# Performance work log

Measured on AMD Instinct MI355X. Metric: run time of the kernel, lower is better.

## Reference

```python
import jax, jax.numpy as jnp
import numpy as np

N_HEADS = 16
HEAD_DIM = 64
ATTN_WINDOW = 128
ROPE_BASE = 10000.0


def _rotate_half(x):
    # (x0, x1) -> (-x1, x0) over interleaved pairs in the last dim
    xr = x.reshape(*x.shape[:-1], -1, 2)
    out = jnp.stack((-xr[..., 1], xr[..., 0]), axis=-1)
    return out.reshape(x.shape)


def _rope_cos_sin(T, rotary_dim, base, dtype):
    inv_freq = 1.0 / (base ** (jnp.arange(0, rotary_dim, 2, dtype=jnp.float32) / rotary_dim))
    t = jnp.arange(T, dtype=jnp.float32)
    freqs = t[:, None] * inv_freq[None, :]            # (T, rotary_dim/2)
    cos = jnp.repeat(jnp.cos(freqs), 2, axis=-1)      # (T, rotary_dim)
    sin = jnp.repeat(jnp.sin(freqs), 2, axis=-1)
    return cos.astype(dtype), sin.astype(dtype)


def _apply_rope(x, cos, sin):
    # x: (B, H, T, Dh); rotary_dim == Dh here (rope_fraction = 1.0)
    c = cos[None, None, :, :]
    s = sin[None, None, :, :]
    return x * c + _rotate_half(x) * s


def setup_inputs() -> dict:
    key = jax.random.key(0)
    ks = jax.random.split(key, 5)
    B, T, C = 2, 2048, 1024
    x = jax.random.normal(ks[0], (B, T, C), dtype=jnp.float32)
    Wqkv = jax.random.normal(ks[1], (C, 3 * C), dtype=jnp.float32) * 0.02
    bqkv = jax.random.normal(ks[2], (3 * C,), dtype=jnp.float32) * 0.02
    Wproj = jax.random.normal(ks[3], (C, C), dtype=jnp.float32) * 0.02
    bproj = jax.random.normal(ks[4], (C,), dtype=jnp.float32) * 0.02
    return {"x": x, "Wqkv": Wqkv, "bqkv": bqkv, "Wproj": Wproj, "bproj": bproj}


def reference(x, Wqkv, bqkv, Wproj, bproj):
    B, T, C = x.shape
    H, Dh = N_HEADS, HEAD_DIM

    qkv = x @ Wqkv + bqkv                              # (B, T, 3C)
    q, k, v = jnp.split(qkv, 3, axis=-1)

    def heads(t):
        return t.reshape(B, T, H, Dh).transpose(0, 2, 1, 3)  # (B, H, T, Dh)
    q, k, v = heads(q), heads(k), heads(v)

    cos, sin = _rope_cos_sin(T, Dh, ROPE_BASE, x.dtype)
    q = _apply_rope(q, cos, sin)
    k = _apply_rope(k, cos, sin)

    # local causal mask: allowed iff 0 <= i - j < attn_window
    idx = jnp.arange(T)
    rel = idx[:, None] - idx[None, :]
    allowed = (rel >= 0) & (rel < ATTN_WINDOW)         # (T, T)

    scale = 1.0 / jnp.sqrt(jnp.asarray(Dh, dtype=x.dtype))
    scores = jnp.einsum("bhqd,bhkd->bhqk", q, k) * scale
    scores = jnp.where(allowed[None, None], scores, jnp.asarray(-jnp.inf, dtype=x.dtype))
    attn = jax.nn.softmax(scores, axis=-1)
    attn_out = jnp.einsum("bhqk,bhkd->bhqd", attn, v)  # (B, H, T, Dh)

    attn_out = attn_out.transpose(0, 2, 1, 3).reshape(B, T, C)
    return attn_out @ Wproj + bproj
```

## Files before the change

kernel.cpp:

```cpp
#include <hip/hip_runtime.h>


using bf16x8 = short  __attribute__((ext_vector_type(8)));
using f32x4  = float __attribute__((ext_vector_type(4)));

__device__ __forceinline__ float bf2f(unsigned short u) {
    return __uint_as_float(((unsigned int)u) << 16);
}
__device__ __forceinline__ unsigned short f2bf(float f) {
    unsigned int u = __float_as_uint(f);
    u += 0x7fffu + ((u >> 16) & 1u);
    return (unsigned short)(u >> 16);
}

__device__ __forceinline__ void gload_lds16(const unsigned short* g,
                                            unsigned short* l) {
    __builtin_amdgcn_global_load_lds(
        (const __attribute__((address_space(1))) unsigned int*)(g),
        (__attribute__((address_space(3))) unsigned int*)(l),
        16, 0, 0);
}

template <int N>
__device__ __forceinline__ void vm_wait() {
    static_assert(N == 0 || N == 2 || N == 3 || N == 4 || N == 6, "add case");
    if constexpr (N == 0)      asm volatile("s_waitcnt vmcnt(0)" ::: "memory");
    else if constexpr (N == 2) asm volatile("s_waitcnt vmcnt(2)" ::: "memory");
    else if constexpr (N == 3) asm volatile("s_waitcnt vmcnt(3)" ::: "memory");
    else if constexpr (N == 4) asm volatile("s_waitcnt vmcnt(4)" ::: "memory");
    else                       asm volatile("s_waitcnt vmcnt(6)" ::: "memory");
}
__device__ __forceinline__ void lgkm_wait0() {
    asm volatile("s_waitcnt lgkmcnt(0)" ::: "memory");
}

__global__ __launch_bounds__(256) void prep_kernel(
        const float* __restrict__ Wqkv, const float* __restrict__ Wproj,
        const float* __restrict__ x,
        unsigned short* __restrict__ WqkvT, unsigned short* __restrict__ WprojT,
        unsigned short* __restrict__ xb, float* __restrict__ tab) {
    __shared__ unsigned short tile[32][33];
    int blk = blockIdx.x;
    int tid = threadIdx.x;
    if (blk < 4096) {
        const float* W; unsigned short* WT; int cols, bx, by;
        if (blk < 3072) { W = Wqkv;  WT = WqkvT;  cols = 3072; bx = blk % 96; by = blk / 96; }
        else            { W = Wproj; WT = WprojT; cols = 1024; bx = (blk - 3072) & 31; by = (blk - 3072) >> 5; }
        int c0 = bx * 32, r0 = by * 32;
        int tx = tid & 31, ty = tid >> 5;
        for (int i = ty; i < 32; i += 8)
            tile[i][tx] = f2bf(W[(size_t)(r0 + i) * cols + c0 + tx]);
        __syncthreads();
        for (int i = ty; i < 32; i += 8)
            WT[(size_t)(c0 + i) * 1024 + r0 + tx] = tile[tx][i];
    } else if (blk < 5120) {
        for (int i = (blk - 4096) * 256 + tid; i < 1048576; i += 262144) {
            float4 v = ((const float4*)x)[i];
            ushort4 o;
            o.x = f2bf(v.x); o.y = f2bf(v.y); o.z = f2bf(v.z); o.w = f2bf(v.w);
            ((ushort4*)xb)[i] = o;
        }
    } else {
        int idx = (blk - 5120) * 256 + tid;
        int t = idx >> 5, i = idx & 31;
        float inv = powf(10000.0f, -(float)i / 32.0f);
        float ang = (float)t * inv;
        tab[idx * 2]     = cosf(ang);
        tab[idx * 2 + 1] = sinf(ang);
    }
}

template <int BM, int BN, int WM, int WN, bool OUT_BF16, bool FUSE_ROPE, int DEPTH>
__global__ __launch_bounds__(256) void gemm_lds(
        const unsigned short* __restrict__ A,
        const unsigned short* __restrict__ Bt,
        const float* __restrict__ bias,
        void* __restrict__ Cv,
        const float* __restrict__ tab,
        int M, int N, int K) {
    constexpr int MI = BM / 16;
    constexpr int NI = BN / 16;
    constexpr int PW = (MI + NI) / 4;
    constexpr int WGN = BN / WN;
    constexpr int MR = WM / 16, NR = WN / 16;

    __shared__ unsigned short smem[DEPTH * (BM + BN) * 32];
    auto As = [&](int buf) { return &smem[buf * (BM + BN) * 32]; };
    auto Bs = [&](int buf) { return &smem[buf * (BM + BN) * 32 + BM * 32]; };

    int nwg = gridDim.x * gridDim.y;
    int lid = blockIdx.y * gridDim.x + blockIdx.x;
    int orig = (lid & 7) * (nwg >> 3) + (lid >> 3);
    int bx = orig % gridDim.x, by = orig / gridDim.x;

    int row0 = by * BM, col0 = bx * BN;
    int tid = threadIdx.x;
    int lane = tid & 63, wid = tid >> 6;
    int wr = wid / WGN, wc = wid % WGN;
    int fr = lane & 15, kq = lane >> 4;
    int r_in = lane >> 2;
    int scg8 = (((lane & 3) ^ ((lane >> 3) & 3))) * 8;
    int kqs8 = (kq ^ ((fr >> 1) & 3)) * 8;

    f32x4 acc[MR][NR];
    #pragma unroll
    for (int i = 0; i < MR; ++i)
        #pragma unroll
        for (int j = 0; j < NR; ++j)
            acc[i][j] = (f32x4){0.f, 0.f, 0.f, 0.f};

    auto stage = [&](int buf, int kt) {
        #pragma unroll
        for (int t = 0; t < PW; ++t) {
            int j = wid * PW + t;
            if (j < MI) {
                int row = j * 16 + r_in;
                gload_lds16(A + (size_t)(row0 + row) * K + kt + scg8,
                            As(buf) + j * 512);
            } else {
                int jb = j - MI;
                int row = jb * 16 + r_in;
                gload_lds16(Bt + (size_t)(col0 + row) * K + kt + scg8,
                            Bs(buf) + jb * 512);
            }
        }
    };
    auto compute = [&](int buf) {
        bf16x8 af[MR], bfv[NR];
        #pragma unroll
        for (int i = 0; i < MR; ++i)
            af[i] = *(const bf16x8*)&As(buf)[(wr * WM + i * 16 + fr) * 32 + kqs8];
        #pragma unroll
        for (int j = 0; j < NR; ++j)
            bfv[j] = *(const bf16x8*)&Bs(buf)[(wc * WN + j * 16 + fr) * 32 + kqs8];
        #pragma unroll
        for (int i = 0; i < MR; ++i)
            #pragma unroll
            for (int j = 0; j < NR; ++j)
                acc[i][j] = __builtin_amdgcn_mfma_f32_16x16x32_bf16(
                                af[i], bfv[j], acc[i][j], 0, 0, 0);
    };

    int nt = K >> 5;
    stage(0, 0);
    if constexpr (DEPTH == 3) stage(1, 32);
    int cc = 0;
    int cs = DEPTH - 1;
    for (int t = 0; t < nt; ++t) {
        int rem = nt - 1 - t;
        if (rem >= DEPTH - 1) {
            stage(cs, (t + DEPTH - 1) << 5);
            vm_wait<(DEPTH - 1) * PW>();
        } else if (rem == 1) {
            vm_wait<PW>();
        } else {
            vm_wait<0>();
        }
        __builtin_amdgcn_s_barrier();
        compute(cc);
        if (t + 1 < nt) {
            lgkm_wait0();
            __builtin_amdgcn_s_barrier();
        }
        cc = (cc + 1 == DEPTH) ? 0 : cc + 1;
        cs = (cs + 1 == DEPTH) ? 0 : cs + 1;
    }

    int rg = kq * 4;
    if constexpr (OUT_BF16) {
        static_assert(BM * BN <= DEPTH * (BM + BN) * 32, "epilogue tile must fit");
        unsigned short* Ct = smem;
        __syncthreads();
        #pragma unroll
        for (int j = 0; j < NR; ++j) {
            int colL = wc * WN + j * 16 + fr;
            float bz = bias[col0 + colL];
            #pragma unroll
            for (int i = 0; i < MR; ++i) {
                float v4[4];
                #pragma unroll
                for (int r = 0; r < 4; ++r) v4[r] = acc[i][j][r] + bz;
                if constexpr (FUSE_ROPE) {
                    if (col0 < 2048) {
                        int ii2 = (colL & 63) >> 1;
                        bool odd = fr & 1;
                        #pragma unroll
                        for (int r = 0; r < 4; ++r) {
                            float part = __shfl_xor(v4[r], 1);
                            int trow = (row0 + wr * WM + i * 16 + rg + r) & 2047;
                            float cc2 = tab[(trow * 32 + ii2) * 2];
                            float ss = tab[(trow * 32 + ii2) * 2 + 1];
                            v4[r] = odd ? fmaf(v4[r], cc2,  part * ss)
                                        : fmaf(v4[r], cc2, -part * ss);
                        }
                    }
                }
                #pragma unroll
                for (int r = 0; r < 4; ++r)
                    Ct[(wr * WM + i * 16 + rg + r) * BN + colL] = f2bf(v4[r]);
            }
        }
        __syncthreads();
        unsigned short* C = (unsigned short*)Cv;
        constexpr int ROUNDS = (BM * BN / 8) / 256;
        #pragma unroll
        for (int p = 0; p < ROUNDS; ++p) {
            int idx = p * 256 + tid;
            int row = idx / (BN / 8);
            int c8v = (idx % (BN / 8)) * 8;
            *(bf16x8*)&C[(size_t)(row0 + row) * N + col0 + c8v] =
                *(const bf16x8*)&Ct[row * BN + c8v];
        }
    } else {
        float* C = (float*)Cv;
        #pragma unroll
        for (int j = 0; j < NR; ++j) {
            int col = col0 + wc * WN + j * 16 + fr;
            float bz = bias[col];
            #pragma unroll
            for (int i = 0; i < MR; ++i) {
                #pragma unroll
                for (int r = 0; r < 4; ++r) {
                    int row = row0 + wr * WM + i * 16 + rg + r;
                    C[(size_t)row * N + col] = acc[i][j][r] + bz;
                }
            }
        }
    }
}

#define VTS 200
#define PSS 168

__global__ __launch_bounds__(256) void attn_kernel(
        const unsigned short* __restrict__ qkv, unsigned short* __restrict__ aout) {
    __shared__ unsigned short Vt[64 * VTS];
    __shared__ unsigned short Ps[4 * 16 * PSS];

    int bid = blockIdx.x;
    int h  = bid & 15;
    int qt = (bid >> 4) & 31;
    int b  = bid >> 9;
    int Q0 = qt * 64;
    int kbase = Q0 - 127; if (kbase < 0) kbase = 0;
    int nk = Q0 + 64 - kbase;
    int tid = threadIdx.x;

    {
        int r32 = tid & 31;
        int c8  = (tid >> 5) * 8;
        #pragma unroll
        for (int p = 0; p < 7; ++p) {
            int r = p * 32 + r32;
            if (r < VTS) {
                unsigned int wv[4] = {0u, 0u, 0u, 0u};
                if (r < nk) {
                    uint4 v = *(const uint4*)(qkv +
                        (size_t)(b * 2048 + kbase + r) * 3072 + 2048 + h * 64 + c8);
                    wv[0] = v.x; wv[1] = v.y; wv[2] = v.z; wv[3] = v.w;
                }
                #pragma unroll
                for (int j = 0; j < 4; ++j) {
                    Vt[(c8 + 2 * j)     * VTS + r] = (unsigned short)(wv[j] & 0xffffu);
                    Vt[(c8 + 2 * j + 1) * VTS + r] = (unsigned short)(wv[j] >> 16);
                }
            }
        }
    }
    __syncthreads();

    int lane = tid & 63, w = tid >> 6;
    int qw0 = Q0 + w * 16;
    int lo = lane & 15, hi = lane >> 4;

    const unsigned short* qg =
        qkv + (size_t)(b * 2048 + qw0 + lo) * 3072 + h * 64 + hi * 8;
    bf16x8 aq0 = *(const bf16x8*)qg;
    bf16x8 aq1 = *(const bf16x8*)(qg + 32);

    int klo = qw0 - 127; if (klo < kbase) klo = kbase;
    int t0 = (klo - kbase) >> 4;
    int t1 = (qw0 + 15 - kbase) >> 4;
    int ntiles = t1 - t0 + 1;
    if ((ntiles & 1) && t0 > 0) { --t0; ++ntiles; }
    int nks = (ntiles + 1) >> 1;
    int wkb = t0 * 16;

    f32x4 s[10];
    #pragma unroll
    for (int i = 0; i < 10; ++i) s[i] = (f32x4){0.f, 0.f, 0.f, 0.f};
    #pragma unroll
    for (int i = 0; i < 10; ++i) {
        if (i < ntiles) {
            const unsigned short* kg = qkv +
                (size_t)(b * 2048 + kbase + (t0 + i) * 16 + lo) * 3072
                + 1024 + h * 64 + hi * 8;
            bf16x8 bk0 = *(const bf16x8*)kg;
            bf16x8 bk1 = *(const bf16x8*)(kg + 32);
            __builtin_amdgcn_s_setprio(1);
            s[i] = __builtin_amdgcn_mfma_f32_16x16x32_bf16(aq0, bk0, s[i], 0, 0, 0);
            s[i] = __builtin_amdgcn_mfma_f32_16x16x32_bf16(aq1, bk1, s[i], 0, 0, 0);
            __builtin_amdgcn_s_setprio(0);
        }
    }

    const float scale = 0.125f;
    float mx[4] = {-1e30f, -1e30f, -1e30f, -1e30f};
    #pragma unroll
    for (int i = 0; i < 10; ++i) {
        if (i < ntiles) {
            int ka = kbase + (t0 + i) * 16 + lo;
            #pragma unroll
            for (int r = 0; r < 4; ++r) {
                int rel = (qw0 + hi * 4 + r) - ka;
                bool ok = (rel >= 0) && (rel < 128);
                float v = ok ? s[i][r] * scale : -1e30f;
                s[i][r] = v;
                mx[r] = fmaxf(mx[r], v);
            }
        }
    }
    #pragma unroll
    for (int r = 0; r < 4; ++r)
        #pragma unroll
        for (int o = 1; o < 16; o <<= 1)
            mx[r] = fmaxf(mx[r], __shfl_xor(mx[r], o));

    float sum[4] = {0.f, 0.f, 0.f, 0.f};
    #pragma unroll
    for (int i = 0; i < 10; ++i) {
        if (i < ntiles) {
            #pragma unroll
            for (int r = 0; r < 4; ++r) {
                float e = __expf(s[i][r] - mx[r]);
                s[i][r] = e;
                sum[r] += e;
            }
        }
    }
    #pragma unroll
    for (int r = 0; r < 4; ++r) {
        #pragma unroll
        for (int o = 1; o < 16; o <<= 1)
            sum[r] += __shfl_xor(sum[r], o);
        sum[r] = 1.0f / sum[r];
    }

    unsigned short* pw = &Ps[(w * 16) * PSS];
    #pragma unroll
    for (int i = 0; i < 10; ++i) {
        if (i < ntiles) {
            #pragma unroll
            for (int r = 0; r < 4; ++r)
                pw[(hi * 4 + r) * PSS + i * 16 + lo] = f2bf(s[i][r] * sum[r]);
        }
    }
    if (ntiles & 1) {
        int zr = lane >> 2, zc = ntiles * 16 + (lane & 3) * 4;
        *(ushort4*)&pw[zr * PSS + zc] = (ushort4){0, 0, 0, 0};
    }

    f32x4 o[4];
    #pragma unroll
    for (int dt = 0; dt < 4; ++dt) o[dt] = (f32x4){0.f, 0.f, 0.f, 0.f};
    #pragma unroll
    for (int ks = 0; ks < 5; ++ks) {
        if (ks < nks) {
            bf16x8 pa = *(const bf16x8*)&Ps[(w * 16 + lo) * PSS + ks * 32 + hi * 8];
            __builtin_amdgcn_s_setprio(1);
            #pragma unroll
            for (int dt = 0; dt < 4; ++dt) {
                bf16x8 vb = *(const bf16x8*)&Vt[(dt * 16 + lo) * VTS
                                                + wkb + ks * 32 + hi * 8];
                o[dt] = __builtin_amdgcn_mfma_f32_16x16x32_bf16(pa, vb, o[dt], 0, 0, 0);
            }
            __builtin_amdgcn_s_setprio(0);
        }
    }

    #pragma unroll
    for (int dt = 0; dt < 4; ++dt)
        #pragma unroll
        for (int r = 0; r < 4; ++r)
            aout[(size_t)(b * 2048 + qw0 + hi * 4 + r) * 1024
                 + h * 64 + dt * 16 + lo] = f2bf(o[dt][r]);
}

extern "C" void kernel_launch(void* const* d_in, const int* in_sizes, int n_in,
                              void* d_out, int out_size, void* d_ws, size_t ws_size,
                              hipStream_t stream) {
    const float* x     = (const float*)d_in[0];
    const float* Wqkv  = (const float*)d_in[1];
    const float* bqkv  = (const float*)d_in[2];
    const float* Wproj = (const float*)d_in[3];
    const float* bproj = (const float*)d_in[4];
    float* out = (float*)d_out;

    char* ws = (char*)d_ws;
    unsigned short* WqkvT  = (unsigned short*)(ws);
    unsigned short* WprojT = (unsigned short*)(ws + 6291456);
    unsigned short* xb     = (unsigned short*)(ws + 8388608);
    unsigned short* qkv    = (unsigned short*)(ws + 16777216);
    float*          tab    = (float*)        (ws + 41943040);
    unsigned short* attno  = (unsigned short*)(ws + 42467328);

    prep_kernel<<<5376, 256, 0, stream>>>(Wqkv, Wproj, x, WqkvT, WprojT, xb, tab);

    gemm_lds<128, 64, 32, 64, true, true, 2>
        <<<dim3(48, 32), 256, 0, stream>>>(xb, WqkvT, bqkv, qkv, tab, 4096, 3072, 1024);
    attn_kernel<<<1024, 256, 0, stream>>>(qkv, attno);
    gemm_lds<64, 64, 32, 32, false, false, 2>
        <<<dim3(16, 64), 256, 0, stream>>>(attno, WprojT, bproj, out, nullptr, 4096, 1024, 1024);
}
```

Measured before the change: 114.5 us.

## Add direct-A-load 128x128 QKV GEMM and enlarge projection GEMM tiles

Adds a dedicated QKV GEMM kernel with 128x128 tiles. Each wave loads its A fragments straight from global memory into registers, and only B is staged through LDS with double-buffered async loads. This halves the number of QKV workgroups and raises per-wave MFMA reuse (4x4 fragments). It also moves the output projection GEMM from 64x64 to 128x64 tiles, and removes the now-unused bf16/RoPE epilogue from the generic template. The cost is uncoalesced-per-lane A global loads that are not shared across waves, plus fewer workgroups (768 and 512) to fill the GPU.

```diff
diff --git a/kernel.cpp b/kernel.cpp
--- a/kernel.cpp
+++ b/kernel.cpp
@@ -70,13 +70,129 @@
     }
 }
 
-template <int BM, int BN, int WM, int WN, bool OUT_BF16, bool FUSE_ROPE, int DEPTH>
+__global__ __launch_bounds__(256) void gemm1_adirect(
+        const unsigned short* __restrict__ A,
+        const unsigned short* __restrict__ Bt,
+        const float* __restrict__ bias,
+        unsigned short* __restrict__ C,
+        const float* __restrict__ tab,
+        int M, int N, int K) {
+    __shared__ unsigned short smem[128 * 128];
+    auto Bs = [&](int buf) { return &smem[buf * 128 * 32]; };
+
+    int nwg = gridDim.x * gridDim.y;
+    int lid = blockIdx.y * gridDim.x + blockIdx.x;
+    int orig = (lid & 7) * (nwg >> 3) + (lid >> 3);
+    int bx = orig % gridDim.x, by = orig / gridDim.x;
+    int row0 = by * 128, col0 = bx * 128;
+
+    int tid = threadIdx.x;
+    int lane = tid & 63, wid = tid >> 6;
+    int wr = wid >> 1, wc = wid & 1;
+    int fr = lane & 15, kq = lane >> 4;
+    int r_in = lane >> 2;
+    int scg8 = (((lane & 3) ^ ((lane >> 3) & 3))) * 8;
+    int kqs8 = (kq ^ ((fr >> 1) & 3)) * 8;
+
+    f32x4 acc[4][4];
+    #pragma unroll
+    for (int i = 0; i < 4; ++i)
+        #pragma unroll
+        for (int j = 0; j < 4; ++j)
+            acc[i][j] = (f32x4){0.f, 0.f, 0.f, 0.f};
+
+    auto stageB = [&](int buf, int kt) {
+        #pragma unroll
+        for (int t = 0; t < 2; ++t) {
+            int jb = wid * 2 + t;
+            int row = jb * 16 + r_in;
+            gload_lds16(Bt + (size_t)(col0 + row) * K + kt + scg8,
+                        Bs(buf) + jb * 512);
+        }
+    };
+
+    const unsigned short* Arow =
+        A + (size_t)(row0 + wr * 64 + fr) * K + kq * 8;
+
+    int nt = K >> 5;
+    stageB(0, 0);
+    for (int t = 0; t < nt; ++t) {
+        int kt = t << 5;
+        bf16x8 af[4];
+        #pragma unroll
+        for (int i = 0; i < 4; ++i)
+            af[i] = *(const bf16x8*)(Arow + (size_t)(i * 16) * K + kt);
+        __builtin_amdgcn_sched_barrier(0);
+        if (t + 1 < nt) {
+            stageB((t + 1) & 1, kt + 32);
+            vm_wait<6>();
+        } else {
+            vm_wait<4>();
+        }
+        __builtin_amdgcn_s_barrier();
+        bf16x8 bfv[4];
+        #pragma unroll
+        for (int j = 0; j < 4; ++j)
+            bfv[j] = *(const bf16x8*)&Bs(t & 1)[(wc * 64 + j * 16 + fr) * 32 + kqs8];
+        #pragma unroll
+        for (int i = 0; i < 4; ++i)
+            #pragma unroll
+            for (int j = 0; j < 4; ++j)
+                acc[i][j] = __builtin_amdgcn_mfma_f32_16x16x32_bf16(
+                                af[i], bfv[j], acc[i][j], 0, 0, 0);
+        if (t + 1 < nt) {
+            lgkm_wait0();
+            __builtin_amdgcn_s_barrier();
+        }
+    }
+
+    int rg = kq * 4;
+    unsigned short* Ct = smem;
+    __syncthreads();
+    #pragma unroll
+    for (int j = 0; j < 4; ++j) {
+        int colL = wc * 64 + j * 16 + fr;
+        float bz = bias[col0 + colL];
+        #pragma unroll
+        for (int i = 0; i < 4; ++i) {
+            float v4[4];
+            #pragma unroll
+            for (int r = 0; r < 4; ++r) v4[r] = acc[i][j][r] + bz;
+            if (col0 < 2048) {
+                int ii2 = (colL & 63) >> 1;
+                bool odd = fr & 1;
+                #pragma unroll
+                for (int r = 0; r < 4; ++r) {
+                    float part = __shfl_xor(v4[r], 1);
+                    int trow = (row0 + wr * 64 + i * 16 + rg + r) & 2047;
+                    float cc2 = tab[(trow * 32 + ii2) * 2];
+                    float ss = tab[(trow * 32 + ii2) * 2 + 1];
+                    v4[r] = odd ? fmaf(v4[r], cc2,  part * ss)
+                                : fmaf(v4[r], cc2, -part * ss);
+                }
+            }
+            #pragma unroll
+            for (int r = 0; r < 4; ++r)
+                Ct[(wr * 64 + i * 16 + rg + r) * 128 + colL] = f2bf(v4[r]);
+        }
+    }
+    __syncthreads();
+    #pragma unroll
+    for (int p = 0; p < 8; ++p) {
+        int idx = p * 256 + tid;
+        int row = idx >> 4;
+        int c8v = (idx & 15) * 8;
+        *(bf16x8*)&C[(size_t)(row0 + row) * N + col0 + c8v] =
+            *(const bf16x8*)&Ct[row * 128 + c8v];
+    }
+}
+
+template <int BM, int BN, int WM, int WN, bool OUT_BF16, int DEPTH>
 __global__ __launch_bounds__(256) void gemm_lds(
         const unsigned short* __restrict__ A,
         const unsigned short* __restrict__ Bt,
         const float* __restrict__ bias,
         void* __restrict__ Cv,
-        const float* __restrict__ tab,
         int M, int N, int K) {
     constexpr int MI = BM / 16;
     constexpr int NI = BN / 16;
@@ -144,8 +260,7 @@
     int nt = K >> 5;
     stage(0, 0);
     if constexpr (DEPTH == 3) stage(1, 32);
-    int cc = 0;
-    int cs = DEPTH - 1;
+    int cc = 0, cs = DEPTH - 1;
     for (int t = 0; t < nt; ++t) {
         int rem = nt - 1 - t;
         if (rem >= DEPTH - 1) {
@@ -167,63 +282,17 @@
     }
 
     int rg = kq * 4;
-    if constexpr (OUT_BF16) {
-        static_assert(BM * BN <= DEPTH * (BM + BN) * 32, "epilogue tile must fit");
-        unsigned short* Ct = smem;
-        __syncthreads();
-        #pragma unroll
-        for (int j = 0; j < NR; ++j) {
-            int colL = wc * WN + j * 16 + fr;
-            float bz = bias[col0 + colL];
-            #pragma unroll
-            for (int i = 0; i < MR; ++i) {
-                float v4[4];
-                #pragma unroll
-                for (int r = 0; r < 4; ++r) v4[r] = acc[i][j][r] + bz;
-                if constexpr (FUSE_ROPE) {
-                    if (col0 < 2048) {
-                        int ii2 = (colL & 63) >> 1;
-                        bool odd = fr & 1;
-                        #pragma unroll
-                        for (int r = 0; r < 4; ++r) {
-                            float part = __shfl_xor(v4[r], 1);
-                            int trow = (row0 + wr * WM + i * 16 + rg + r) & 2047;
-                            float cc2 = tab[(trow * 32 + ii2) * 2];
-                            float ss = tab[(trow * 32 + ii2) * 2 + 1];
-                            v4[r] = odd ? fmaf(v4[r], cc2,  part * ss)
-                                        : fmaf(v4[r], cc2, -part * ss);
-                        }
-                    }
-                }
-                #pragma unroll
-                for (int r = 0; r < 4; ++r)
-                    Ct[(wr * WM + i * 16 + rg + r) * BN + colL] = f2bf(v4[r]);
-            }
-        }
-        __syncthreads();
-        unsigned short* C = (unsigned short*)Cv;
-        constexpr int ROUNDS = (BM * BN / 8) / 256;
-        #pragma unroll
-        for (int p = 0; p < ROUNDS; ++p) {
-            int idx = p * 256 + tid;
-            int row = idx / (BN / 8);
-            int c8v = (idx % (BN / 8)) * 8;
-            *(bf16x8*)&C[(size_t)(row0 + row) * N + col0 + c8v] =
-                *(const bf16x8*)&Ct[row * BN + c8v];
-        }
-    } else {
-        float* C = (float*)Cv;
-        #pragma unroll
-        for (int j = 0; j < NR; ++j) {
-            int col = col0 + wc * WN + j * 16 + fr;
-            float bz = bias[col];
-            #pragma unroll
-            for (int i = 0; i < MR; ++i) {
-                #pragma unroll
-                for (int r = 0; r < 4; ++r) {
-                    int row = row0 + wr * WM + i * 16 + rg + r;
-                    C[(size_t)row * N + col] = acc[i][j][r] + bz;
-                }
+    float* C = (float*)Cv;
+    #pragma unroll
+    for (int j = 0; j < NR; ++j) {
+        int col = col0 + wc * WN + j * 16 + fr;
+        float bz = bias[col];
+        #pragma unroll
+        for (int i = 0; i < MR; ++i) {
+            #pragma unroll
+            for (int r = 0; r < 4; ++r) {
+                int row = row0 + wr * WM + i * 16 + rg + r;
+                C[(size_t)row * N + col] = acc[i][j][r] + bz;
             }
         }
     }
@@ -406,9 +475,9 @@
 
     prep_kernel<<<5376, 256, 0, stream>>>(Wqkv, Wproj, x, WqkvT, WprojT, xb, tab);
 
-    gemm_lds<128, 64, 32, 64, true, true, 2>
-        <<<dim3(48, 32), 256, 0, stream>>>(xb, WqkvT, bqkv, qkv, tab, 4096, 3072, 1024);
+    gemm1_adirect<<<dim3(24, 32), 256, 0, stream>>>(
+        xb, WqkvT, bqkv, qkv, tab, 4096, 3072, 1024);
     attn_kernel<<<1024, 256, 0, stream>>>(qkv, attno);
-    gemm_lds<64, 64, 32, 32, false, false, 2>
-        <<<dim3(16, 64), 256, 0, stream>>>(attno, WprojT, bproj, out, nullptr, 4096, 1024, 1024);
-}
+    gemm_lds<128, 64, 32, 64, false, 2>
+        <<<dim3(16, 32), 256, 0, stream>>>(attno, WprojT, bproj, out, 4096, 1024, 1024);
+}
```

Result: slower. 120.0 us (+4.7%).
